# Performance work log

Hardware: AMD Instinct MI355X
Metric: run time of the kernel (lower is better)

Reference implementation:

```python
import jax, jax.numpy as jnp
import numpy as np

B = 16          # patients
V = 30          # max_visit
NV = 1501       # num_nodes + 1 (node vocab incl. padding)
NE = 2001       # num_edges + 1 (relation vocab incl. padding)
H = 128         # hidden_dim
D = 128         # start_embed_dim
L = 2           # gnn layers
OUT = 25        # out_dim
N_TOTAL = 100000  # concatenated graph nodes
E = 800000        # concatenated graph edges
DECAY = 0.01
EPS = 0.0       # self_attn


def setup_inputs() -> dict:
    key = jax.random.key(0)
    ks = jax.random.split(key, 16)
    s = 0.02
    return dict(
        node_emb_w=jax.random.normal(ks[0], (NV, D), jnp.float32) * s,
        edge_emb_w=jax.random.normal(ks[1], (NE, D), jnp.float32) * s,
        lin_w=jax.random.normal(ks[2], (H, D), jnp.float32) * s,
        lin_b=jnp.zeros((H,), jnp.float32),
        alpha_w=jax.random.normal(ks[3], (L, NV, NV), jnp.float32) * 0.01,
        alpha_b=jnp.zeros((L, NV), jnp.float32),
        beta_w=jax.random.normal(ks[4], (L, 1, NV), jnp.float32) * 0.01,
        beta_b=jnp.zeros((L, 1), jnp.float32),
        wr_w=jax.random.normal(ks[5], (L, 1, H), jnp.float32) * s,
        wr_b=jnp.zeros((L, 1), jnp.float32),
        conv_w=jax.random.normal(ks[6], (L, H, H), jnp.float32) * s,
        conv_b=jnp.zeros((L, H), jnp.float32),
        mlp_w=jax.random.normal(ks[7], (OUT, 2 * H), jnp.float32) * s,
        mlp_b=jnp.zeros((OUT,), jnp.float32),
        visit_node=jax.random.randint(ks[8], (B, V, NV), 0, 2).astype(jnp.int32),
        ehr_nodes=jax.random.randint(ks[9], (B, NV), 0, 2).astype(jnp.int32),
        cat_node_ids=jax.random.randint(ks[10], (N_TOTAL,), 1, NV).astype(jnp.int32),
        cat_edge_ids=jax.random.randint(ks[11], (E,), 1, NE).astype(jnp.int32),
        edge_index=jax.random.randint(ks[12], (2, E), 0, N_TOTAL).astype(jnp.int32),
        batch=jnp.repeat(jnp.arange(B, dtype=jnp.int32), N_TOTAL // B),
    )


def reference(node_emb_w, edge_emb_w, lin_w, lin_b, alpha_w, alpha_b,
              beta_w, beta_b, wr_w, wr_b, conv_w, conv_b, mlp_w, mlp_b,
              visit_node, ehr_nodes, cat_node_ids, cat_edge_ids, edge_index, batch):
    # lambda_j = exp(decay * (max_visit - j)), shape [1, V, 1]
    lam = jnp.exp(DECAY * (V - jnp.arange(V, dtype=jnp.float32)))[None, :, None]
    # embedding lookup + shared linear projection
    x = node_emb_w[cat_node_ids] @ lin_w.T + lin_b          # [N_total, H]
    eattr = edge_emb_w[cat_edge_ids] @ lin_w.T + lin_b      # [E, H]
    vn = visit_node.astype(jnp.float32)                     # [B, V, NV]
    src, dst = edge_index[0], edge_index[1]
    xj_nid = cat_node_ids[src]                               # [E]
    xj_b = batch[src]                                        # [E]
    for l in range(L):
        # visit-level attention: softmax over visits (dim=1)
        alpha = jax.nn.softmax(vn @ alpha_w[l].T + alpha_b[l], axis=1)   # [B,V,NV]
        beta = jnp.tanh(vn @ beta_w[l].T + beta_b[l]) * lam              # [B,V,1]
        attn = jnp.sum(alpha * beta, axis=1)                              # [B,NV]
        e_attn = attn[xj_b, xj_nid][:, None]                              # [E,1] per-edge gather
        # BiAttentionGNNConv: message = relu(x_j * attn * sigmoid(W_R e)), aggr=add
        w_rel = jax.nn.sigmoid(eattr @ wr_w[l].T + wr_b[l])               # [E,1]
        msg = jax.nn.relu(x[src] * e_attn * w_rel)                        # [E,H]
        agg = jax.ops.segment_sum(msg, dst, num_segments=N_TOTAL)        # scatter-add
        x = jax.nn.relu((agg + (1.0 + EPS) * x) @ conv_w[l].T + conv_b[l])
    # global mean pool over batch segments
    counts = jax.ops.segment_sum(jnp.ones((N_TOTAL,), jnp.float32), batch, num_segments=B)
    x_graph = jax.ops.segment_sum(x, batch, num_segments=B) / counts[:, None]
    # node branch: multi-hot average of node embeddings, then shared lin
    ehr = ehr_nodes.astype(jnp.float32)
    x_node = (ehr @ node_emb_w) / jnp.sum(ehr, axis=1, keepdims=True)
    x_node = x_node @ lin_w.T + lin_b
    return jnp.concatenate([x_graph, x_node], axis=1) @ mlp_w.T + mlp_b  # [B, OUT]
```

## Files before the change

kernel.cpp:

```cpp
#include <hip/hip_runtime.h>
#include <math.h>

namespace {
constexpr int kB = 16, kV = 30, kNV = 1501, kNE = 2001, kH = 128, kD = 128,
              kL = 2, kOut = 25, kNT = 100000, kE = 800000, kM = kB * kV;
constexpr int kKP = 1504;
constexpr int kKSZ = 4;
constexpr int kNVZ = 1536;
constexpr int kMZ = 512;
constexpr int kCAP = 32;
}

typedef __attribute__((ext_vector_type(8))) short bfrag;
typedef __attribute__((ext_vector_type(4))) float ffrag;

__device__ inline unsigned short f2bf(float x) {
  unsigned u = __float_as_uint(x);
  unsigned r = u + 0x7FFFu + ((u >> 16) & 1u);
  return (unsigned short)(r >> 16);
}
__device__ inline float bf2f(unsigned short h) {
  return __uint_as_float(((unsigned)h) << 16);
}

__global__ void pn_kernel(const float* __restrict__ emb, const float* __restrict__ lw,
                          const float* __restrict__ lb, const float* __restrict__ cw,
                          const float* __restrict__ cb, float* __restrict__ pn,
                          float* __restrict__ pq2, float* __restrict__ ps,
                          float* __restrict__ accz) {
  int n = blockIdx.x, h = threadIdx.x;
  if (n == 0) {
    for (int i = h; i < 4128; i += kH) accz[i] = 0.f;
  }
  __shared__ float erow[kD];
  __shared__ float row[kD];
  erow[h] = emb[(size_t)n * kD + h];
  __syncthreads();
  float acc = lb[h];
#pragma unroll 8
  for (int d = 0; d < kD; d++) acc += erow[d] * lw[h * kD + d];
  pn[(size_t)n * kH + h] = acc;
  row[h] = acc;
  __syncthreads();
  float ap = 0.f, am = 0.f, aps = cb[h];
  const float* wr = cw + h * kD;
#pragma unroll 8
  for (int d = 0; d < kD; d++) {
    float r = row[d];
    float w = wr[d];
    ap = fmaf(fmaxf(r, 0.f), w, ap);
    am = fmaf(fmaxf(-r, 0.f), w, am);
    aps = fmaf(r, w, aps);
  }
  pq2[(size_t)n * kH + h] = ap;
  pq2[(size_t)(kNV + n) * kH + h] = am;
  ps[(size_t)n * kH + h] = aps;
}

__global__ void xnode_kernel(const int* __restrict__ ehr, const float* __restrict__ pn,
                             float* __restrict__ xacc, int* __restrict__ cnte) {
  int b = blockIdx.x;
  int c = blockIdx.y;
  int h = threadIdx.x;
  int n0 = c * 128;
  __shared__ int flags[128];
  int gn = n0 + h;
  flags[h] = (gn < kNV) ? ehr[(size_t)b * kNV + gn] : 0;
  __syncthreads();
  float acc = 0.f;
  int cnt = 0;
  int n1 = min(n0 + 128, kNV);
  for (int n = n0; n < n1; ++n) {
    if (flags[n - n0]) {
      acc += pn[(size_t)n * kH + h];
      cnt++;
    }
  }
  atomicAdd(&xacc[b * kH + h], acc);
  if (h == 0) atomicAdd(&cnte[b], cnt);
}

__global__ void wrel_kernel(const float* __restrict__ eemb, const float* __restrict__ wrw,
                            const float* __restrict__ wrb, const float* __restrict__ lw,
                            const float* __restrict__ lb, float* __restrict__ wrel) {
  __shared__ float uc[258];
  int t = threadIdx.x;
  {
    int l = t >> 7, d = t & 127;
    float s = 0.f;
    for (int h = 0; h < kH; h++) s += wrw[l * kH + h] * lw[h * kD + d];
    uc[t] = s;
    if (t < kL) {
      float c = wrb[t];
      for (int h = 0; h < kH; h++) c += wrw[t * kH + h] * lb[h];
      uc[256 + t] = c;
    }
  }
  __syncthreads();
  int idx = blockIdx.x * blockDim.x + t;
  if (idx >= kL * kNE) return;
  int l = idx / kNE, r = idx % kNE;
  float z = uc[256 + l];
  const float* u = uc + l * 128;
  const float* er = eemb + (size_t)r * kD;
  for (int d = 0; d < kD; d++) z += er[d] * u[d];
  wrel[idx] = 1.f / (1.f + expf(-z));
}

__global__ void vnbf_kernel(const int* __restrict__ vn, short* __restrict__ out,
                            int* __restrict__ curz, const int* __restrict__ batch,
                            int* __restrict__ cnt, const float* __restrict__ bw,
                            const float* __restrict__ bb, float* __restrict__ beta) {
  int m = blockIdx.x;
  int b = m >> 5, v = m & 31;
  int tid = threadIdx.x;
  int gidx = blockIdx.x * 256 + tid;
  for (int i = gidx; i < 200000; i += 512 * 256) curz[i] = 0;
  __shared__ int bh[kB];
  __shared__ float rs[2][256];
  if (tid < kB) bh[tid] = 0;
  __syncthreads();
  if (gidx < kNT) atomicAdd(&bh[batch[gidx]], 1);
  __syncthreads();
  if (tid < kB && bh[tid]) atomicAdd(&cnt[tid], bh[tid]);
  float s0 = 0.f, s1 = 0.f;
  for (int k = tid; k < kKP; k += 256) {
    int val = (v < kV && k < kNV) ? vn[((size_t)(b * kV + v)) * kNV + k] : 0;
    out[(size_t)m * kKP + k] = val ? (short)0x3F80 : (short)0;
    if (val) {
      s0 += bw[k];
      s1 += bw[kNV + k];
    }
  }
  rs[0][tid] = s0;
  rs[1][tid] = s1;
  __syncthreads();
  for (int o = 128; o > 0; o >>= 1) {
    if (tid < o) {
      rs[0][tid] += rs[0][tid + o];
      rs[1][tid] += rs[1][tid + o];
    }
    __syncthreads();
  }
  if (tid == 0 && v < kV) {
    float lam = expf(0.01f * (float)(kV - v));
    beta[b * kV + v] = tanhf(rs[0][0] + bb[0]) * lam;
    beta[kM + b * kV + v] = tanhf(rs[1][0] + bb[1]) * lam;
  }
}

__global__ void awsplit_kernel(const float* __restrict__ aw, short* __restrict__ awh) {
  int n = blockIdx.x;
  int l = blockIdx.y;
  const size_t pl = (size_t)kKP * kKP;
  size_t rowo = ((size_t)l * kKP + n) * kKP;
  for (int k = threadIdx.x; k < kKP; k += 256) {
    float x = (n < kNV && k < kNV) ? aw[((size_t)l * kNV + n) * kNV + k] : 0.f;
    unsigned short h1 = f2bf(x);
    float r1 = x - bf2f(h1);
    unsigned short h2 = f2bf(r1);
    float r2 = r1 - bf2f(h2);
    unsigned short h3 = f2bf(r2);
    awh[rowo + k] = (short)h1;
    awh[2 * pl + rowo + k] = (short)h2;
    awh[4 * pl + rowo + k] = (short)h3;
  }
}

__global__ void zmfma_kernel(const short* __restrict__ vnbf, const short* __restrict__ awh,
                             float* __restrict__ zp) {
  const int l = blockIdx.z >> 2, ks = blockIdx.z & 3;
  const int wv = threadIdx.x >> 6, lane = threadIdx.x & 63;
  const int m0 = (blockIdx.y * 4 + wv) * 64;
  const int n0 = blockIdx.x * 32;
  const int lrow = lane & 15;
  const int koff = (lane >> 4) * 8;
  const size_t pl = (size_t)kKP * kKP;
  const short* p0 = awh + ((size_t)0 * 2 + l) * pl;
  const short* p1 = awh + ((size_t)1 * 2 + l) * pl;
  const short* p2 = awh + ((size_t)2 * 2 + l) * pl;
  ffrag acc[4][2];
#pragma unroll
  for (int i = 0; i < 4; ++i)
#pragma unroll
    for (int j = 0; j < 2; ++j) acc[i][j] = ffrag{0.f, 0.f, 0.f, 0.f};
  const int ct0 = ks * 12;
  const int ct1 = min(ct0 + 12, 47);
  for (int kt = ct0; kt < ct1; ++kt) {
    const int k = kt * 32 + koff;
    bfrag a0 = *(const bfrag*)(vnbf + (size_t)(m0 + 0 * 16 + lrow) * kKP + k);
    bfrag a1 = *(const bfrag*)(vnbf + (size_t)(m0 + 1 * 16 + lrow) * kKP + k);
    bfrag a2 = *(const bfrag*)(vnbf + (size_t)(m0 + 2 * 16 + lrow) * kKP + k);
    bfrag a3 = *(const bfrag*)(vnbf + (size_t)(m0 + 3 * 16 + lrow) * kKP + k);
    {
      bfrag b0 = *(const bfrag*)(p0 + (size_t)(n0 + lrow) * kKP + k);
      bfrag b1 = *(const bfrag*)(p0 + (size_t)(n0 + 16 + lrow) * kKP + k);
      acc[0][0] = __builtin_amdgcn_mfma_f32_16x16x32_bf16(a0, b0, acc[0][0], 0, 0, 0);
      acc[1][0] = __builtin_amdgcn_mfma_f32_16x16x32_bf16(a1, b0, acc[1][0], 0, 0, 0);
      acc[2][0] = __builtin_amdgcn_mfma_f32_16x16x32_bf16(a2, b0, acc[2][0], 0, 0, 0);
      acc[3][0] = __builtin_amdgcn_mfma_f32_16x16x32_bf16(a3, b0, acc[3][0], 0, 0, 0);
      acc[0][1] = __builtin_amdgcn_mfma_f32_16x16x32_bf16(a0, b1, acc[0][1], 0, 0, 0);
      acc[1][1] = __builtin_amdgcn_mfma_f32_16x16x32_bf16(a1, b1, acc[1][1], 0, 0, 0);
      acc[2][1] = __builtin_amdgcn_mfma_f32_16x16x32_bf16(a2, b1, acc[2][1], 0, 0, 0);
      acc[3][1] = __builtin_amdgcn_mfma_f32_16x16x32_bf16(a3, b1, acc[3][1], 0, 0, 0);
    }
    {
      bfrag b0 = *(const bfrag*)(p1 + (size_t)(n0 + lrow) * kKP + k);
      bfrag b1 = *(const bfrag*)(p1 + (size_t)(n0 + 16 + lrow) * kKP + k);
      acc[0][0] = __builtin_amdgcn_mfma_f32_16x16x32_bf16(a0, b0, acc[0][0], 0, 0, 0);
      acc[1][0] = __builtin_amdgcn_mfma_f32_16x16x32_bf16(a1, b0, acc[1][0], 0, 0, 0);
      acc[2][0] = __builtin_amdgcn_mfma_f32_16x16x32_bf16(a2, b0, acc[2][0], 0, 0, 0);
      acc[3][0] = __builtin_amdgcn_mfma_f32_16x16x32_bf16(a3, b0, acc[3][0], 0, 0, 0);
      acc[0][1] = __builtin_amdgcn_mfma_f32_16x16x32_bf16(a0, b1, acc[0][1], 0, 0, 0);
      acc[1][1] = __builtin_amdgcn_mfma_f32_16x16x32_bf16(a1, b1, acc[1][1], 0, 0, 0);
      acc[2][1] = __builtin_amdgcn_mfma_f32_16x16x32_bf16(a2, b1, acc[2][1], 0, 0, 0);
      acc[3][1] = __builtin_amdgcn_mfma_f32_16x16x32_bf16(a3, b1, acc[3][1], 0, 0, 0);
    }
    {
      bfrag b0 = *(const bfrag*)(p2 + (size_t)(n0 + lrow) * kKP + k);
      bfrag b1 = *(const bfrag*)(p2 + (size_t)(n0 + 16 + lrow) * kKP + k);
      acc[0][0] = __builtin_amdgcn_mfma_f32_16x16x32_bf16(a0, b0, acc[0][0], 0, 0, 0);
      acc[1][0] = __builtin_amdgcn_mfma_f32_16x16x32_bf16(a1, b0, acc[1][0], 0, 0, 0);
      acc[2][0] = __builtin_amdgcn_mfma_f32_16x16x32_bf16(a2, b0, acc[2][0], 0, 0, 0);
      acc[3][0] = __builtin_amdgcn_mfma_f32_16x16x32_bf16(a3, b0, acc[3][0], 0, 0, 0);
      acc[0][1] = __builtin_amdgcn_mfma_f32_16x16x32_bf16(a0, b1, acc[0][1], 0, 0, 0);
      acc[1][1] = __builtin_amdgcn_mfma_f32_16x16x32_bf16(a1, b1, acc[1][1], 0, 0, 0);
      acc[2][1] = __builtin_amdgcn_mfma_f32_16x16x32_bf16(a2, b1, acc[2][1], 0, 0, 0);
      acc[3][1] = __builtin_amdgcn_mfma_f32_16x16x32_bf16(a3, b1, acc[3][1], 0, 0, 0);
    }
  }
  const int drow0 = (lane >> 4) * 4;
  float* zb = zp + (size_t)(ks * kL + l) * kMZ * kNVZ;
#pragma unroll
  for (int i = 0; i < 4; ++i) {
    int mrow = m0 + i * 16 + drow0;
#pragma unroll
    for (int j = 0; j < 2; ++j) {
      int ncol = n0 + j * 16 + lrow;
#pragma unroll
      for (int r = 0; r < 4; ++r) zb[(size_t)(mrow + r) * kNVZ + ncol] = acc[i][j][r];
    }
  }
}

__global__ void zsm_kernel(const float* __restrict__ zp, const float* __restrict__ beta,
                           float* __restrict__ attn) {
  int idx = blockIdx.x * blockDim.x + threadIdx.x;
  if (idx >= kL * kB * kNV) return;
  int n = idx % kNV;
  int lb_ = idx / kNV;
  int l = lb_ / kB, b = lb_ % kB;
  const size_t PSTR = (size_t)kL * kMZ * kNVZ;
  const float* p = zp + ((size_t)l * kMZ + b * 32) * kNVZ + n;
  float zz[kV];
  float m = -1e30f;
#pragma unroll
  for (int v = 0; v < kV; ++v) {
    size_t o = (size_t)v * kNVZ;
    float s = p[o] + p[o + PSTR] + p[o + 2 * PSTR] + p[o + 3 * PSTR];
    zz[v] = s;
    m = fmaxf(m, s);
  }
  float s = 0.f, num = 0.f;
  const float* bet = beta + lb_ * kV;
#pragma unroll
  for (int v = 0; v < kV; ++v) {
    float e = expf(zz[v] - m);
    s += e;
    num += e * bet[v];
  }
  attn[idx] = num / s;
}

__global__ void scatter_kernel(const int* __restrict__ ei, const int* __restrict__ nid,
                               const int* __restrict__ eid, const int* __restrict__ batch,
                               const float* __restrict__ attn, const float* __restrict__ wrel,
                               int* __restrict__ cnt1, unsigned short* __restrict__ csnb,
                               float* __restrict__ cs0b, int* __restrict__ cnt2,
                               int* __restrict__ csrs2b, float* __restrict__ cs1cb) {
  int e = blockIdx.x * blockDim.x + threadIdx.x;
  if (e >= kE) return;
  int s = ei[e], d = ei[kE + e];
  int b = batch[s], n = nid[s], r = eid[e];
  float a0 = attn[(size_t)b * kNV + n];
  float a1 = attn[(size_t)kB * kNV + b * kNV + n];
  float w0 = wrel[r], w1 = wrel[kNE + r];
  int pos = atomicAdd(&cnt1[d], 1);
  if (pos < kCAP) {
    csnb[(size_t)d * kCAP + pos] = (unsigned short)(n + ((a0 > 0.f) ? 0 : kNV));
    cs0b[(size_t)d * kCAP + pos] = fabsf(a0) * w0;
  }
  if (a1 > 0.f) {
    int p2 = atomicAdd(&cnt2[d], 1);
    if (p2 < kCAP) {
      csrs2b[(size_t)d * kCAP + p2] = s;
      cs1cb[(size_t)d * kCAP + p2] = a1 * w1;
    }
  }
}

#define GACC(A, V, C)                                  \
  A.x = fmaf(V.x, C, A.x); A.y = fmaf(V.y, C, A.y);    \
  A.z = fmaf(V.z, C, A.z); A.w = fmaf(V.w, C, A.w);

__global__ void l1_kernel(const float* __restrict__ pq2, const float* __restrict__ psTab,
                          const int* __restrict__ nid, const unsigned short* __restrict__ csn,
                          const float* __restrict__ cs0, const int* __restrict__ cnt1,
                          float* __restrict__ xa) {
  const int tid = threadIdx.x;
  const int lane = tid & 63;
  const int sub = lane >> 5, sl = lane & 31;
  const int hw = (tid >> 6) * 2 + sub;
  int node = blockIdx.x * 16 + hw;
  if (node >= kNT) return;
  const float4* x4 = (const float4*)pq2;
  float4 a0 = ((const float4*)psTab)[(size_t)nid[node] * 32 + sl];
  float4 a1 = {0.f, 0.f, 0.f, 0.f};
  float4 a2 = {0.f, 0.f, 0.f, 0.f};
  float4 a3 = {0.f, 0.f, 0.f, 0.f};
  int j0 = node * kCAP;
  int j1 = j0 + min(cnt1[node], kCAP);
  for (int base = j0; base < j1; base += 32) {
    int n = j1 - base;
    if (n > 32) n = 32;
    int sidx = 0;
    float ssc = 0.f;
    if (sl < n) {
      sidx = (int)csn[base + sl];
      ssc = cs0[base + sl];
    }
    int t = 0;
    for (; t + 8 <= n; t += 8) {
      int s0 = __shfl(sidx, sub * 32 + t + 0, 64);
      int s1 = __shfl(sidx, sub * 32 + t + 1, 64);
      int s2 = __shfl(sidx, sub * 32 + t + 2, 64);
      int s3 = __shfl(sidx, sub * 32 + t + 3, 64);
      int s4i = __shfl(sidx, sub * 32 + t + 4, 64);
      int s5 = __shfl(sidx, sub * 32 + t + 5, 64);
      int s6 = __shfl(sidx, sub * 32 + t + 6, 64);
      int s7 = __shfl(sidx, sub * 32 + t + 7, 64);
      float c0 = __shfl(ssc, sub * 32 + t + 0, 64);
      float c1 = __shfl(ssc, sub * 32 + t + 1, 64);
      float c2 = __shfl(ssc, sub * 32 + t + 2, 64);
      float c3 = __shfl(ssc, sub * 32 + t + 3, 64);
      float c4 = __shfl(ssc, sub * 32 + t + 4, 64);
      float c5 = __shfl(ssc, sub * 32 + t + 5, 64);
      float c6 = __shfl(ssc, sub * 32 + t + 6, 64);
      float c7 = __shfl(ssc, sub * 32 + t + 7, 64);
      float4 v0 = x4[(size_t)s0 * 32 + sl];
      float4 v1 = x4[(size_t)s1 * 32 + sl];
      float4 v2 = x4[(size_t)s2 * 32 + sl];
      float4 v3 = x4[(size_t)s3 * 32 + sl];
      float4 v4 = x4[(size_t)s4i * 32 + sl];
      float4 v5 = x4[(size_t)s5 * 32 + sl];
      float4 v6 = x4[(size_t)s6 * 32 + sl];
      float4 v7 = x4[(size_t)s7 * 32 + sl];
      GACC(a0, v0, c0);
      GACC(a1, v1, c1);
      GACC(a2, v2, c2);
      GACC(a3, v3, c3);
      GACC(a0, v4, c4);
      GACC(a1, v5, c5);
      GACC(a2, v6, c6);
      GACC(a3, v7, c7);
    }
    for (; t + 4 <= n; t += 4) {
      int s0 = __shfl(sidx, sub * 32 + t + 0, 64);
      int s1 = __shfl(sidx, sub * 32 + t + 1, 64);
      int s2 = __shfl(sidx, sub * 32 + t + 2, 64);
      int s3 = __shfl(sidx, sub * 32 + t + 3, 64);
      float c0 = __shfl(ssc, sub * 32 + t + 0, 64);
      float c1 = __shfl(ssc, sub * 32 + t + 1, 64);
      float c2 = __shfl(ssc, sub * 32 + t + 2, 64);
      float c3 = __shfl(ssc, sub * 32 + t + 3, 64);
      float4 v0 = x4[(size_t)s0 * 32 + sl];
      float4 v1 = x4[(size_t)s1 * 32 + sl];
      float4 v2 = x4[(size_t)s2 * 32 + sl];
      float4 v3 = x4[(size_t)s3 * 32 + sl];
      GACC(a0, v0, c0);
      GACC(a1, v1, c1);
      GACC(a2, v2, c2);
      GACC(a3, v3, c3);
    }
    for (; t < n; ++t) {
      int s = __shfl(sidx, sub * 32 + t, 64);
      float sc = __shfl(ssc, sub * 32 + t, 64);
      float4 xv = x4[(size_t)s * 32 + sl];
      GACC(a0, xv, sc);
    }
  }
  float4 o;
  o.x = fmaxf(a0.x + a1.x + a2.x + a3.x, 0.f);
  o.y = fmaxf(a0.y + a1.y + a2.y + a3.y, 0.f);
  o.z = fmaxf(a0.z + a1.z + a2.z + a3.z, 0.f);
  o.w = fmaxf(a0.w + a1.w + a2.w + a3.w, 0.f);
  ((float4*)xa)[(size_t)node * 32 + sl] = o;
}

template <int POOL>
__global__ void gconv_kernel(const float* __restrict__ srcTab,
                             const float* __restrict__ selfTab,
                             const int* __restrict__ cidx, const float* __restrict__ cscal,
                             const int* __restrict__ cnt, const int* __restrict__ selfIdx,
                             const float* __restrict__ w, const float* __restrict__ bias,
                             float* __restrict__ xout, float* __restrict__ xg,
                             const int* __restrict__ batch) {
  const int nb = blockIdx.x * 64;
  const int tid = threadIdx.x;
  __shared__ float As[128 * 64];
  __shared__ float Ws[32 * 132];
  const int wv = tid >> 6;
  const int lane = tid & 63;
  const int sub = lane >> 5, sl = lane & 31;
  const int hw = wv * 2 + sub;
  const float4* x4 = (const float4*)srcTab;
  const float4* s4 = (const float4*)selfTab;
  int nct[4];
  int sidxr[4];
  float sscr[4];
  float4 selfa[4];
#pragma unroll
  for (int p = 0; p < 4; ++p) {
    int node = nb + p * 16 + hw;
    if (node < kNT) {
      size_t jb = (size_t)node * kCAP;
      nct[p] = cnt[node];
      sidxr[p] = cidx[jb + sl];
      sscr[p] = cscal[jb + sl];
      int selfRow = selfIdx ? selfIdx[node] : node;
      selfa[p] = s4[(size_t)selfRow * 32 + sl];
    } else {
      nct[p] = 0;
      sidxr[p] = 0;
      sscr[p] = 0.f;
      selfa[p] = float4{0.f, 0.f, 0.f, 0.f};
    }
  }
#pragma unroll
  for (int p = 0; p < 4; ++p) {
    int nl = p * 16 + hw;
    int node = nb + nl;
    if (node < kNT) {
      float4 a0 = selfa[p];
      float4 a1 = {0.f, 0.f, 0.f, 0.f};
      float4 a2 = {0.f, 0.f, 0.f, 0.f};
      float4 a3 = {0.f, 0.f, 0.f, 0.f};
      int n = min(nct[p], kCAP);
      int sidx = sidxr[p];
      float ssc = sscr[p];
      int t = 0;
      for (; t + 8 <= n; t += 8) {
        int s0 = __shfl(sidx, sub * 32 + t + 0, 64);
        int s1 = __shfl(sidx, sub * 32 + t + 1, 64);
        int s2 = __shfl(sidx, sub * 32 + t + 2, 64);
        int s3 = __shfl(sidx, sub * 32 + t + 3, 64);
        int s4i = __shfl(sidx, sub * 32 + t + 4, 64);
        int s5 = __shfl(sidx, sub * 32 + t + 5, 64);
        int s6 = __shfl(sidx, sub * 32 + t + 6, 64);
        int s7 = __shfl(sidx, sub * 32 + t + 7, 64);
        float c0 = __shfl(ssc, sub * 32 + t + 0, 64);
        float c1 = __shfl(ssc, sub * 32 + t + 1, 64);
        float c2 = __shfl(ssc, sub * 32 + t + 2, 64);
        float c3 = __shfl(ssc, sub * 32 + t + 3, 64);
        float c4 = __shfl(ssc, sub * 32 + t + 4, 64);
        float c5 = __shfl(ssc, sub * 32 + t + 5, 64);
        float c6 = __shfl(ssc, sub * 32 + t + 6, 64);
        float c7 = __shfl(ssc, sub * 32 + t + 7, 64);
        float4 v0 = x4[(size_t)s0 * 32 + sl];
        float4 v1 = x4[(size_t)s1 * 32 + sl];
        float4 v2 = x4[(size_t)s2 * 32 + sl];
        float4 v3 = x4[(size_t)s3 * 32 + sl];
        float4 v4 = x4[(size_t)s4i * 32 + sl];
        float4 v5 = x4[(size_t)s5 * 32 + sl];
        float4 v6 = x4[(size_t)s6 * 32 + sl];
        float4 v7 = x4[(size_t)s7 * 32 + sl];
        GACC(a0, v0, c0);
        GACC(a1, v1, c1);
        GACC(a2, v2, c2);
        GACC(a3, v3, c3);
        GACC(a0, v4, c4);
        GACC(a1, v5, c5);
        GACC(a2, v6, c6);
        GACC(a3, v7, c7);
      }
      for (; t + 4 <= n; t += 4) {
        int s0 = __shfl(sidx, sub * 32 + t + 0, 64);
        int s1 = __shfl(sidx, sub * 32 + t + 1, 64);
        int s2 = __shfl(sidx, sub * 32 + t + 2, 64);
        int s3 = __shfl(sidx, sub * 32 + t + 3, 64);
        float c0 = __shfl(ssc, sub * 32 + t + 0, 64);
        float c1 = __shfl(ssc, sub * 32 + t + 1, 64);
        float c2 = __shfl(ssc, sub * 32 + t + 2, 64);
        float c3 = __shfl(ssc, sub * 32 + t + 3, 64);
        float4 v0 = x4[(size_t)s0 * 32 + sl];
        float4 v1 = x4[(size_t)s1 * 32 + sl];
        float4 v2 = x4[(size_t)s2 * 32 + sl];
        float4 v3 = x4[(size_t)s3 * 32 + sl];
        GACC(a0, v0, c0);
        GACC(a1, v1, c1);
        GACC(a2, v2, c2);
        GACC(a3, v3, c3);
      }
      for (; t < n; ++t) {
        int s = __shfl(sidx, sub * 32 + t, 64);
        float sc = __shfl(ssc, sub * 32 + t, 64);
        float4 xv = x4[(size_t)s * 32 + sl];
        GACC(a0, xv, sc);
      }
      float av[4] = {a0.x + a1.x + a2.x + a3.x, a0.y + a1.y + a2.y + a3.y,
                     a0.z + a1.z + a2.z + a3.z, a0.w + a1.w + a2.w + a3.w};
#pragma unroll
      for (int j = 0; j < 4; ++j) {
        int d = sl * 4 + j;
        int g = (nl >> 2) ^ (sl & 15);
        As[d * 64 + (g << 2) + (nl & 3)] = av[j];
      }
    }
  }
  __syncthreads();
  const int tx = tid & 31, ty = tid >> 5;
  const int n0 = tx * 4;
  float acc[4][4] = {};
  for (int kc = 0; kc < 4; ++kc) {
    if (kc) __syncthreads();
#pragma unroll
    for (int i = 0; i < 2; ++i) {
      int fi = tid + i * 512;
      int hh = fi >> 3, c4 = (fi & 7) * 4;
      float4 v = *(const float4*)(w + (size_t)hh * kD + kc * 32 + c4);
      Ws[(c4 + 0) * 132 + hh] = v.x;
      Ws[(c4 + 1) * 132 + hh] = v.y;
      Ws[(c4 + 2) * 132 + hh] = v.z;
      Ws[(c4 + 3) * 132 + hh] = v.w;
    }
    __syncthreads();
#pragma unroll
    for (int dd = 0; dd < 32; ++dd) {
      int d = kc * 32 + dd;
      float4 a = *(const float4*)&As[d * 64 + ((ty ^ ((d >> 2) & 15)) << 2)];
      float4 b0 = *(const float4*)&Ws[dd * 132 + n0];
      float am[4] = {a.x, a.y, a.z, a.w};
      float bn[4] = {b0.x, b0.y, b0.z, b0.w};
#pragma unroll
      for (int i2 = 0; i2 < 4; ++i2)
#pragma unroll
        for (int j2 = 0; j2 < 4; ++j2) acc[i2][j2] += am[i2] * bn[j2];
    }
  }
  float4 bv0 = *(const float4*)(bias + n0);
  float bb[4] = {bv0.x, bv0.y, bv0.z, bv0.w};
  if (POOL == 0) {
#pragma unroll
    for (int i2 = 0; i2 < 4; ++i2) {
      int r = nb + ty * 4 + i2;
      if (r < kNT) {
        float4 o0;
        o0.x = fmaxf(acc[i2][0] + bb[0], 0.f);
        o0.y = fmaxf(acc[i2][1] + bb[1], 0.f);
        o0.z = fmaxf(acc[i2][2] + bb[2], 0.f);
        o0.w = fmaxf(acc[i2][3] + bb[3], 0.f);
        *(float4*)(xout + (size_t)r * kH + n0) = o0;
      }
    }
  } else {
    int rlast = min(nb + 63, kNT - 1);
    int b0 = batch[nb], b1v = batch[rlast];
    if (b0 == b1v) {
      float p[4] = {};
#pragma unroll
      for (int i2 = 0; i2 < 4; ++i2) {
        int r = nb + ty * 4 + i2;
        if (r < kNT) {
#pragma unroll
          for (int j2 = 0; j2 < 4; ++j2) p[j2] += fmaxf(acc[i2][j2] + bb[j2], 0.f);
        }
      }
      __syncthreads();
      float* Ls = Ws;
#pragma unroll
      for (int j2 = 0; j2 < 4; ++j2) Ls[ty * 132 + n0 + j2] = p[j2];
      __syncthreads();
      if (tid < 128) {
        float s = 0.f;
#pragma unroll
        for (int r2 = 0; r2 < 16; ++r2) s += Ls[r2 * 132 + tid];
        atomicAdd(&xg[b0 * kH + tid], s);
      }
    } else {
#pragma unroll
      for (int i2 = 0; i2 < 4; ++i2) {
        int r = nb + ty * 4 + i2;
        if (r < kNT) {
          int br = batch[r];
#pragma unroll
          for (int j2 = 0; j2 < 4; ++j2)
            atomicAdd(&xg[br * kH + n0 + j2], fmaxf(acc[i2][j2] + bb[j2], 0.f));
        }
      }
    }
  }
}

__global__ void final_kernel(const float* __restrict__ xg, const int* __restrict__ cnt,
                             const float* __restrict__ xacc, const int* __restrict__ cnte,
                             const float* __restrict__ mw, const float* __restrict__ mb,
                             float* __restrict__ out) {
  int idx = blockIdx.x * blockDim.x + threadIdx.x;
  if (idx >= kB * kOut) return;
  int b = idx / kOut, o = idx % kOut;
  float invg = 1.f / (float)cnt[b];
  float invn = 1.f / (float)cnte[b];
  float acc = mb[o];
  const float* w = mw + (size_t)o * (2 * kH);
  for (int h = 0; h < kH; h++) acc += xg[b * kH + h] * invg * w[h];
  for (int h = 0; h < kH; h++) acc += xacc[b * kH + h] * invn * w[kH + h];
  out[idx] = acc;
}

extern "C" void kernel_launch(void* const* d_in, const int* in_sizes, int n_in,
                              void* d_out, int out_size, void* d_ws, size_t ws_size,
                              hipStream_t stream) {
  const float* node_emb = (const float*)d_in[0];
  const float* edge_emb = (const float*)d_in[1];
  const float* lin_w = (const float*)d_in[2];
  const float* lin_b = (const float*)d_in[3];
  const float* alpha_w = (const float*)d_in[4];
  const float* alpha_b = (const float*)d_in[5];
  const float* beta_w = (const float*)d_in[6];
  const float* beta_b = (const float*)d_in[7];
  const float* wr_w = (const float*)d_in[8];
  const float* wr_b = (const float*)d_in[9];
  const float* conv_w = (const float*)d_in[10];
  const float* conv_b = (const float*)d_in[11];
  const float* mlp_w = (const float*)d_in[12];
  const float* mlp_b = (const float*)d_in[13];
  const int* visit_node = (const int*)d_in[14];
  const int* ehr_nodes = (const int*)d_in[15];
  const int* cat_node_ids = (const int*)d_in[16];
  const int* cat_edge_ids = (const int*)d_in[17];
  const int* edge_index = (const int*)d_in[18];
  const int* batch = (const int*)d_in[19];

  char* ws = (char*)d_ws;
  float* ZP = (float*)(ws);
  float* XA = (float*)(ws);
  float* PN = (float*)(ws + 51200000);
  short* VNBF = (short*)(ws + 52000000);
  float* PQ2 = (float*)(ws + 53600000);
  float* PS = (float*)(ws + 55200000);
  short* AWH = (short*)(ws + 56000000);
  unsigned short* CSNB = (unsigned short*)(ws + 56000000);
  float* CS0B = (float*)(ws + 62400000);
  float* ATTN = (float*)(ws + 83200000);
  float* BETA = (float*)(ws + 83400000);
  float* WREL = (float*)(ws + 83410000);
  int* CNT1 = (int*)(ws + 83500000);
  int* CNT2 = (int*)(ws + 83900000);
  int* CSRS2B = (int*)(ws + 84300000);
  float* CS1CB = (float*)(ws + 97100000);
  float* XG = (float*)(ws + 109900000);
  int* CNT = (int*)(ws + 109908192);
  float* XNACC = (float*)(ws + 109908256);
  int* CNTE = (int*)(ws + 109916448);

  pn_kernel<<<kNV, kH, 0, stream>>>(node_emb, lin_w, lin_b, conv_w, conv_b, PN, PQ2, PS, XG);
  xnode_kernel<<<dim3(kB, 12), kH, 0, stream>>>(ehr_nodes, PN, XNACC, CNTE);
  wrel_kernel<<<(kL * kNE + 255) / 256, 256, 0, stream>>>(edge_emb, wr_w, wr_b, lin_w, lin_b,
                                                          WREL);
  vnbf_kernel<<<kMZ, 256, 0, stream>>>(visit_node, VNBF, CNT1, batch, CNT, beta_w, beta_b,
                                       BETA);
  awsplit_kernel<<<dim3(kKP, kL), 256, 0, stream>>>(alpha_w, AWH);
  zmfma_kernel<<<dim3(47, 2, kL * kKSZ), 256, 0, stream>>>(VNBF, AWH, ZP);
  zsm_kernel<<<(kL * kB * kNV + 255) / 256, 256, 0, stream>>>(ZP, BETA, ATTN);

  scatter_kernel<<<(kE + 255) / 256, 256, 0, stream>>>(edge_index, cat_node_ids, cat_edge_ids,
                                                       batch, ATTN, WREL, CNT1, CSNB, CS0B,
                                                       CNT2, CSRS2B, CS1CB);

  l1_kernel<<<(kNT + 15) / 16, 512, 0, stream>>>(PQ2, PS, cat_node_ids, CSNB, CS0B, CNT1, XA);
  gconv_kernel<1><<<(kNT + 63) / 64, 512, 0, stream>>>(XA, XA, CSRS2B, CS1CB, CNT2, nullptr,
                                                       conv_w + (size_t)kH * kD, conv_b + kH,
                                                       nullptr, XG, batch);

  final_kernel<<<2, 256, 0, stream>>>(XG, CNT, XNACC, CNTE, mlp_w, mlp_b, (float*)d_out);
}
```

Measured before the change: 304.2 us.

## Halve gconv node tile to 32 and drop register prefetch of neighbor lists

The fused gather+GEMM graph conv kernel now processes 32 nodes per block instead of 64, which halves its shared-memory A tile and doubles the grid size. The up-front prefetch of neighbor indices, scales and self rows into register arrays is removed, and neighbor indices are loaded only for lanes below the neighbor count. The GEMM mapping becomes 2 rows per thread with an adjusted XOR swizzle. This aims to raise occupancy and parallelism in exchange for less memory-level parallelism per wave, half the compute per block, and twice the weight tile reloads and pooling atomics per node.

```diff
diff --git a/kernel.cpp b/kernel.cpp
--- a/kernel.cpp
+++ b/kernel.cpp
@@ -405,9 +405,9 @@
                              const float* __restrict__ w, const float* __restrict__ bias,
                              float* __restrict__ xout, float* __restrict__ xg,
                              const int* __restrict__ batch) {
-  const int nb = blockIdx.x * 64;
+  const int nb = blockIdx.x * 32;
   const int tid = threadIdx.x;
-  __shared__ float As[128 * 64];
+  __shared__ float As[128 * 32];
   __shared__ float Ws[32 * 132];
   const int wv = tid >> 6;
   const int lane = tid & 63;
@@ -415,39 +415,23 @@
   const int hw = wv * 2 + sub;
   const float4* x4 = (const float4*)srcTab;
   const float4* s4 = (const float4*)selfTab;
-  int nct[4];
-  int sidxr[4];
-  float sscr[4];
-  float4 selfa[4];
-#pragma unroll
-  for (int p = 0; p < 4; ++p) {
-    int node = nb + p * 16 + hw;
-    if (node < kNT) {
-      size_t jb = (size_t)node * kCAP;
-      nct[p] = cnt[node];
-      sidxr[p] = cidx[jb + sl];
-      sscr[p] = cscal[jb + sl];
-      int selfRow = selfIdx ? selfIdx[node] : node;
-      selfa[p] = s4[(size_t)selfRow * 32 + sl];
-    } else {
-      nct[p] = 0;
-      sidxr[p] = 0;
-      sscr[p] = 0.f;
-      selfa[p] = float4{0.f, 0.f, 0.f, 0.f};
-    }
-  }
-#pragma unroll
-  for (int p = 0; p < 4; ++p) {
+  for (int p = 0; p < 2; ++p) {
     int nl = p * 16 + hw;
     int node = nb + nl;
     if (node < kNT) {
-      float4 a0 = selfa[p];
+      int selfRow = selfIdx ? selfIdx[node] : node;
+      float4 a0 = s4[(size_t)selfRow * 32 + sl];
       float4 a1 = {0.f, 0.f, 0.f, 0.f};
       float4 a2 = {0.f, 0.f, 0.f, 0.f};
       float4 a3 = {0.f, 0.f, 0.f, 0.f};
-      int n = min(nct[p], kCAP);
-      int sidx = sidxr[p];
-      float ssc = sscr[p];
+      int n = min(cnt[node], kCAP);
+      int sidx = 0;
+      float ssc = 0.f;
+      if (sl < n) {
+        size_t jb = (size_t)node * kCAP;
+        sidx = cidx[jb + sl];
+        ssc = cscal[jb + sl];
+      }
       int t = 0;
       for (; t + 8 <= n; t += 8) {
         int s0 = __shfl(sidx, sub * 32 + t + 0, 64);
@@ -512,15 +496,16 @@
 #pragma unroll
       for (int j = 0; j < 4; ++j) {
         int d = sl * 4 + j;
-        int g = (nl >> 2) ^ (sl & 15);
-        As[d * 64 + (g << 2) + (nl & 3)] = av[j];
+        int g = ((nl >> 2) ^ (sl & 7)) & 7;
+        As[d * 32 + (g << 2) + (nl & 3)] = av[j];
       }
     }
   }
   __syncthreads();
   const int tx = tid & 31, ty = tid >> 5;
   const int n0 = tx * 4;
-  float acc[4][4] = {};
+  const int q = ty >> 1, hp = (ty & 1) * 2;
+  float acc[2][4] = {};
   for (int kc = 0; kc < 4; ++kc) {
     if (kc) __syncthreads();
 #pragma unroll
@@ -537,12 +522,13 @@
 #pragma unroll
     for (int dd = 0; dd < 32; ++dd) {
       int d = kc * 32 + dd;
-      float4 a = *(const float4*)&As[d * 64 + ((ty ^ ((d >> 2) & 15)) << 2)];
+      float4 a = *(const float4*)&As[d * 32 + ((q ^ ((d >> 2) & 7)) << 2)];
+      const float* af = (const float*)&a;
+      float am[2] = {af[hp], af[hp + 1]};
       float4 b0 = *(const float4*)&Ws[dd * 132 + n0];
-      float am[4] = {a.x, a.y, a.z, a.w};
       float bn[4] = {b0.x, b0.y, b0.z, b0.w};
 #pragma unroll
-      for (int i2 = 0; i2 < 4; ++i2)
+      for (int i2 = 0; i2 < 2; ++i2)
 #pragma unroll
         for (int j2 = 0; j2 < 4; ++j2) acc[i2][j2] += am[i2] * bn[j2];
     }
@@ -551,8 +537,8 @@
   float bb[4] = {bv0.x, bv0.y, bv0.z, bv0.w};
   if (POOL == 0) {
 #pragma unroll
-    for (int i2 = 0; i2 < 4; ++i2) {
-      int r = nb + ty * 4 + i2;
+    for (int i2 = 0; i2 < 2; ++i2) {
+      int r = nb + ty * 2 + i2;
       if (r < kNT) {
         float4 o0;
         o0.x = fmaxf(acc[i2][0] + bb[0], 0.f);
@@ -563,22 +549,22 @@
       }
     }
   } else {
-    int rlast = min(nb + 63, kNT - 1);
+    int rlast = min(nb + 31, kNT - 1);
     int b0 = batch[nb], b1v = batch[rlast];
     if (b0 == b1v) {
-      float p[4] = {};
-#pragma unroll
-      for (int i2 = 0; i2 < 4; ++i2) {
-        int r = nb + ty * 4 + i2;
+      float pp[4] = {};
+#pragma unroll
+      for (int i2 = 0; i2 < 2; ++i2) {
+        int r = nb + ty * 2 + i2;
         if (r < kNT) {
 #pragma unroll
-          for (int j2 = 0; j2 < 4; ++j2) p[j2] += fmaxf(acc[i2][j2] + bb[j2], 0.f);
+          for (int j2 = 0; j2 < 4; ++j2) pp[j2] += fmaxf(acc[i2][j2] + bb[j2], 0.f);
         }
       }
       __syncthreads();
       float* Ls = Ws;
 #pragma unroll
-      for (int j2 = 0; j2 < 4; ++j2) Ls[ty * 132 + n0 + j2] = p[j2];
+      for (int j2 = 0; j2 < 4; ++j2) Ls[ty * 132 + n0 + j2] = pp[j2];
       __syncthreads();
       if (tid < 128) {
         float s = 0.f;
@@ -588,8 +574,8 @@
       }
     } else {
 #pragma unroll
-      for (int i2 = 0; i2 < 4; ++i2) {
-        int r = nb + ty * 4 + i2;
+      for (int i2 = 0; i2 < 2; ++i2) {
+        int r = nb + ty * 2 + i2;
         if (r < kNT) {
           int br = batch[r];
 #pragma unroll
@@ -678,7 +664,7 @@
                                                        CNT2, CSRS2B, CS1CB);
 
   l1_kernel<<<(kNT + 15) / 16, 512, 0, stream>>>(PQ2, PS, cat_node_ids, CSNB, CS0B, CNT1, XA);
-  gconv_kernel<1><<<(kNT + 63) / 64, 512, 0, stream>>>(XA, XA, CSRS2B, CS1CB, CNT2, nullptr,
+  gconv_kernel<1><<<(kNT + 31) / 32, 512, 0, stream>>>(XA, XA, CSRS2B, CS1CB, CNT2, nullptr,
                                                        conv_w + (size_t)kH * kD, conv_b + kH,
                                                        nullptr, XG, batch);
 
```

Result: slower. 399.5 us (+31.3%).
